# Optimization experiments

Hardware: AMD Instinct MI355X
Metric: run time of the kernel (lower is better)

Reference implementation:

```python
import jax, jax.numpy as jnp
from jax import lax
import numpy as np

K = 3        # kernel_size
G = 8        # groups
BN_EPS = 1e-5


def setup_inputs() -> dict:
    key = jax.random.key(0)
    k1, k2, k3, k4 = jax.random.split(key, 4)
    N, C, H, W = 16, 256, 128, 128
    x = jax.random.normal(k1, (N, C, H, W), dtype=jnp.float32)
    # grouped conv: out = G*K*K = 72 channels, in-per-group = C/G = 32, OIHW layout
    fan_out = (G * K * K // G) * K * K  # kaiming fan_out per torch convention
    std = np.sqrt(2.0 / fan_out)
    conv_w = jax.random.normal(k2, (G * K * K, C // G, K, K), dtype=jnp.float32) * std
    gamma = jnp.ones((G * K * K,), dtype=jnp.float32)
    beta = jnp.zeros((G * K * K,), dtype=jnp.float32)
    running_mean = jax.random.normal(k3, (G * K * K,), dtype=jnp.float32) * 0.1
    running_var = jax.random.uniform(k4, (G * K * K,), dtype=jnp.float32, minval=0.5, maxval=1.5)
    return {"x": x, "conv_w": conv_w, "gamma": gamma, "beta": beta,
            "running_mean": running_mean, "running_var": running_var}


def reference(x, conv_w, gamma, beta, running_mean, running_var):
    n, c, h, w = x.shape
    # ReflectionPad2d(K//2)
    xp = jnp.pad(x, ((0, 0), (0, 0), (1, 1), (1, 1)), mode="reflect")
    # grouped conv -> per-pixel logits, shape (n, G*K*K, h, w)
    sigma = lax.conv_general_dilated(
        xp, conv_w, window_strides=(1, 1), padding="VALID",
        dimension_numbers=("NCHW", "OIHW", "NCHW"), feature_group_count=G)
    # BatchNorm (inference mode: running stats)
    scale = gamma * lax.rsqrt(running_var + BN_EPS)
    sigma = sigma * scale[None, :, None, None] + (beta - running_mean * scale)[None, :, None, None]
    # softmax over the full channel dim (faithful to nn.Softmax(dim=1) on G*K*K channels)
    sigma = jax.nn.softmax(sigma, axis=1)
    sigma = sigma.reshape(n, G, K * K, h, w)
    # unfold(x_pad, K): 9 shifted views, channel-major then row-major kernel order
    patches = jnp.stack(
        [xp[:, :, i:i + h, j:j + w] for i in range(K) for j in range(K)], axis=2
    )  # (n, c, K*K, h, w)
    patches = patches.reshape(n, G, c // G, K * K, h, w)
    # per-pixel weighted sum over kernel taps, weights shared within each group
    out = jnp.einsum("ngpkhw,ngkhw->ngphw", patches, sigma)
    return out.reshape(n, c, h, w)
```

## Files before the change

### kernel.cpp

```cpp
#include <hip/hip_runtime.h>


#define NN    16
#define CTOT  256
#define HH    128
#define WW    128
#define NG    8
#define CPG   32
#define NCH   72
#define BN_EPS 1e-5f

typedef float f2 __attribute__((ext_vector_type(2)));

__global__ void aaf_prep(const float* __restrict__ gamma,
                         const float* __restrict__ beta,
                         const float* __restrict__ rmean,
                         const float* __restrict__ rvar,
                         float* __restrict__ ws) {
    int t = threadIdx.x;
    if (t < NCH) {
        float sc = gamma[t] * rsqrtf(rvar[t] + BN_EPS);
        ws[t]       = sc;
        ws[NCH + t] = beta[t] - rmean[t] * sc;
    }
}

__global__ __launch_bounds__(512, 4) void aaf_main(
    const float* __restrict__ x,
    const float* __restrict__ wf,
    const float* __restrict__ scale,
    const float* __restrict__ bias,
    float* __restrict__ out) {

    __shared__ float red_m[NG][WW];
    __shared__ float red_s[NG][WW];

    int t = threadIdx.x & 63;
    int g = __builtin_amdgcn_readfirstlane((int)threadIdx.x >> 6);

    int bid = blockIdx.x;
    int row = (bid & 7) * (2048 / 8) + (bid >> 3);
    int n = row >> 7;
    int h = row & 127;

    int ys[3];
    ys[0] = (h == 0)   ? 1   : h - 1;
    ys[1] = h;
    ys[2] = (h == 127) ? 126 : h + 1;

    const float* xg = x + ((size_t)n << 22) + ((size_t)(g * CPG) << 14);
    int w0 = t << 1;

    float sig0[9], sig1[9];
#pragma unroll
    for (int o = 0; o < 9; o++) { sig0[o] = 0.f; sig1[o] = 0.f; }

    for (int ci = 0; ci < CPG; ci++) {
        const float* xc = xg + ((size_t)ci << 14);
        const float* wb = wf + (size_t)(g * 9) * (CPG * 9) + ci * 9;
#pragma unroll
        for (int ky = 0; ky < 3; ky++) {
            f2 ab = *reinterpret_cast<const f2*>(xc + (ys[ky] << 7) + w0);
            float a = ab.x, b = ab.y;
            float l = __shfl_up(b, 1);
            float r = __shfl_down(a, 1);
#pragma unroll
            for (int o = 0; o < 9; o++) {
                float wk0 = wb[o * (CPG * 9) + ky * 3 + 0];
                float wk1 = wb[o * (CPG * 9) + ky * 3 + 1];
                float wk2 = wb[o * (CPG * 9) + ky * 3 + 2];
                sig0[o] = fmaf(l, wk0, fmaf(a, wk1, fmaf(b, wk2, sig0[o])));
                sig1[o] = fmaf(a, wk0, fmaf(b, wk1, fmaf(r, wk2, sig1[o])));
            }
        }
    }

    float m0 = -3.0e38f, m1 = -3.0e38f;
#pragma unroll
    for (int o = 0; o < 9; o++) {
        float sc = scale[g * 9 + o], bi = bias[g * 9 + o];
        sig0[o] = fmaf(sig0[o], sc, bi);
        sig1[o] = fmaf(sig1[o], sc, bi);
        m0 = fmaxf(m0, sig0[o]);
        m1 = fmaxf(m1, sig1[o]);
    }
    float S0 = 0.f, S1 = 0.f;
#pragma unroll
    for (int o = 0; o < 9; o++) {
        sig0[o] = __expf(sig0[o] - m0);
        sig1[o] = __expf(sig1[o] - m1);
        S0 += sig0[o];
        S1 += sig1[o];
    }
    red_m[g][w0]     = m0;
    red_m[g][w0 + 1] = m1;
    red_s[g][w0]     = S0;
    red_s[g][w0 + 1] = S1;

    __syncthreads();
    float d0 = 0.f, d1 = 0.f;
#pragma unroll
    for (int rg = 0; rg < NG; rg++) {
        d0 += red_s[rg][w0]     * __expf(red_m[rg][w0]     - m0);
        d1 += red_s[rg][w0 + 1] * __expf(red_m[rg][w0 + 1] - m1);
    }
    float inv0 = 1.f / d0, inv1 = 1.f / d1;
#pragma unroll
    for (int o = 0; o < 9; o++) { sig0[o] *= inv0; sig1[o] *= inv1; }

    size_t obase = ((size_t)n << 22) + ((size_t)(g * CPG) << 14)
                 + ((size_t)h << 7) + (size_t)w0;
    for (int ci = 0; ci < CPG; ci++) {
        const float* xc = xg + ((size_t)ci << 14);
        float o0 = 0.f, o1 = 0.f;
#pragma unroll
        for (int ky = 0; ky < 3; ky++) {
            f2 ab = *reinterpret_cast<const f2*>(xc + (ys[ky] << 7) + w0);
            float a = ab.x, b = ab.y;
            float l = __shfl_up(b, 1);
            float r = __shfl_down(a, 1);
            o0 = fmaf(l, sig0[ky * 3 + 0], fmaf(a, sig0[ky * 3 + 1], fmaf(b, sig0[ky * 3 + 2], o0)));
            o1 = fmaf(a, sig1[ky * 3 + 0], fmaf(b, sig1[ky * 3 + 1], fmaf(r, sig1[ky * 3 + 2], o1)));
        }
        f2 ov; ov.x = o0; ov.y = o1;
        __builtin_nontemporal_store(ov,
            reinterpret_cast<f2*>(out + obase + ((size_t)ci << 14)));
    }
}

extern "C" void kernel_launch(void* const* d_in, const int* in_sizes, int n_in,
                              void* d_out, int out_size, void* d_ws, size_t ws_size,
                              hipStream_t stream) {
    const float* x     = (const float*)d_in[0];
    const float* cw    = (const float*)d_in[1];
    const float* gamma = (const float*)d_in[2];
    const float* beta  = (const float*)d_in[3];
    const float* rmean = (const float*)d_in[4];
    const float* rvar  = (const float*)d_in[5];
    float* out = (float*)d_out;
    float* ws  = (float*)d_ws;

    hipLaunchKernelGGL(aaf_prep, dim3(1), dim3(128), 0, stream,
                       gamma, beta, rmean, rvar, ws);

    int blocks = NN * HH;
    hipLaunchKernelGGL(aaf_main, dim3(blocks), dim3(512), 0, stream,
                       x, cw, ws, ws + NCH, out);
}
```

Measured before the change: 545.2 us.

## Process four pixels per thread and two rows per block with float4 loads

```diff
diff --git a/kernel.cpp b/kernel.cpp
--- a/kernel.cpp
+++ b/kernel.cpp
@@ -11,6 +11,7 @@
 #define BN_EPS 1e-5f
 
 typedef float f2 __attribute__((ext_vector_type(2)));
+typedef float f4 __attribute__((ext_vector_type(4)));
 
 __global__ void aaf_prep(const float* __restrict__ gamma,
                          const float* __restrict__ beta,
@@ -32,16 +33,19 @@
     const float* __restrict__ bias,
     float* __restrict__ out) {
 
-    __shared__ float red_m[NG][WW];
-    __shared__ float red_s[NG][WW];
+    __shared__ f4 red_m[NG][64];
+    __shared__ f4 red_s[NG][64];
 
-    int t = threadIdx.x & 63;
-    int g = __builtin_amdgcn_readfirstlane((int)threadIdx.x >> 6);
+    int t  = threadIdx.x & 63;
+    int g  = __builtin_amdgcn_readfirstlane((int)threadIdx.x >> 6);
+    int half = t >> 5;
+    int tl   = t & 31;
+    int w0   = tl << 2;
 
     int bid = blockIdx.x;
-    int row = (bid & 7) * (2048 / 8) + (bid >> 3);
-    int n = row >> 7;
-    int h = row & 127;
+    int pr  = (bid & 7) * (1024 / 8) + (bid >> 3);
+    int n   = pr >> 6;
+    int h   = ((pr & 63) << 1) + half;
 
     int ys[3];
     ys[0] = (h == 0)   ? 1   : h - 1;
@@ -49,82 +53,97 @@
     ys[2] = (h == 127) ? 126 : h + 1;
 
     const float* xg = x + ((size_t)n << 22) + ((size_t)(g * CPG) << 14);
-    int w0 = t << 1;
 
-    float sig0[9], sig1[9];
+    float s0[9], s1[9], s2[9], s3[9];
 #pragma unroll
-    for (int o = 0; o < 9; o++) { sig0[o] = 0.f; sig1[o] = 0.f; }
+    for (int o = 0; o < 9; o++) { s0[o] = 0.f; s1[o] = 0.f; s2[o] = 0.f; s3[o] = 0.f; }
 
     for (int ci = 0; ci < CPG; ci++) {
         const float* xc = xg + ((size_t)ci << 14);
         const float* wb = wf + (size_t)(g * 9) * (CPG * 9) + ci * 9;
 #pragma unroll
         for (int ky = 0; ky < 3; ky++) {
-            f2 ab = *reinterpret_cast<const f2*>(xc + (ys[ky] << 7) + w0);
-            float a = ab.x, b = ab.y;
-            float l = __shfl_up(b, 1);
-            float r = __shfl_down(a, 1);
+            f4 v = *reinterpret_cast<const f4*>(xc + (ys[ky] << 7) + w0);
+            float l = __shfl_up(v.w, 1);
+            l = (tl == 0) ? v.y : l;
+            float r = __shfl_down(v.x, 1);
+            r = (tl == 31) ? v.z : r;
 #pragma unroll
             for (int o = 0; o < 9; o++) {
                 float wk0 = wb[o * (CPG * 9) + ky * 3 + 0];
                 float wk1 = wb[o * (CPG * 9) + ky * 3 + 1];
                 float wk2 = wb[o * (CPG * 9) + ky * 3 + 2];
-                sig0[o] = fmaf(l, wk0, fmaf(a, wk1, fmaf(b, wk2, sig0[o])));
-                sig1[o] = fmaf(a, wk0, fmaf(b, wk1, fmaf(r, wk2, sig1[o])));
+                s0[o] = fmaf(l,   wk0, fmaf(v.x, wk1, fmaf(v.y, wk2, s0[o])));
+                s1[o] = fmaf(v.x, wk0, fmaf(v.y, wk1, fmaf(v.z, wk2, s1[o])));
+                s2[o] = fmaf(v.y, wk0, fmaf(v.z, wk1, fmaf(v.w, wk2, s2[o])));
+                s3[o] = fmaf(v.z, wk0, fmaf(v.w, wk1, fmaf(r,   wk2, s3[o])));
             }
         }
     }
 
-    float m0 = -3.0e38f, m1 = -3.0e38f;
+    float m0 = -3.0e38f, m1 = -3.0e38f, m2 = -3.0e38f, m3 = -3.0e38f;
 #pragma unroll
     for (int o = 0; o < 9; o++) {
         float sc = scale[g * 9 + o], bi = bias[g * 9 + o];
-        sig0[o] = fmaf(sig0[o], sc, bi);
-        sig1[o] = fmaf(sig1[o], sc, bi);
-        m0 = fmaxf(m0, sig0[o]);
-        m1 = fmaxf(m1, sig1[o]);
+        s0[o] = fmaf(s0[o], sc, bi);  m0 = fmaxf(m0, s0[o]);
+        s1[o] = fmaf(s1[o], sc, bi);  m1 = fmaxf(m1, s1[o]);
+        s2[o] = fmaf(s2[o], sc, bi);  m2 = fmaxf(m2, s2[o]);
+        s3[o] = fmaf(s3[o], sc, bi);  m3 = fmaxf(m3, s3[o]);
     }
-    float S0 = 0.f, S1 = 0.f;
+    float S0 = 0.f, S1 = 0.f, S2 = 0.f, S3 = 0.f;
 #pragma unroll
     for (int o = 0; o < 9; o++) {
-        sig0[o] = __expf(sig0[o] - m0);
-        sig1[o] = __expf(sig1[o] - m1);
-        S0 += sig0[o];
-        S1 += sig1[o];
+        s0[o] = __expf(s0[o] - m0);  S0 += s0[o];
+        s1[o] = __expf(s1[o] - m1);  S1 += s1[o];
+        s2[o] = __expf(s2[o] - m2);  S2 += s2[o];
+        s3[o] = __expf(s3[o] - m3);  S3 += s3[o];
     }
-    red_m[g][w0]     = m0;
-    red_m[g][w0 + 1] = m1;
-    red_s[g][w0]     = S0;
-    red_s[g][w0 + 1] = S1;
+    {
+        f4 mm; mm.x = m0; mm.y = m1; mm.z = m2; mm.w = m3;
+        f4 ss; ss.x = S0; ss.y = S1; ss.z = S2; ss.w = S3;
+        red_m[g][t] = mm;
+        red_s[g][t] = ss;
+    }
 
     __syncthreads();
-    float d0 = 0.f, d1 = 0.f;
+    float d0 = 0.f, d1 = 0.f, d2 = 0.f, d3 = 0.f;
 #pragma unroll
     for (int rg = 0; rg < NG; rg++) {
-        d0 += red_s[rg][w0]     * __expf(red_m[rg][w0]     - m0);
-        d1 += red_s[rg][w0 + 1] * __expf(red_m[rg][w0 + 1] - m1);
+        f4 mm = red_m[rg][t];
+        f4 ss = red_s[rg][t];
+        d0 += ss.x * __expf(mm.x - m0);
+        d1 += ss.y * __expf(mm.y - m1);
+        d2 += ss.z * __expf(mm.z - m2);
+        d3 += ss.w * __expf(mm.w - m3);
     }
-    float inv0 = 1.f / d0, inv1 = 1.f / d1;
+    float i0 = 1.f / d0, i1 = 1.f / d1, i2 = 1.f / d2, i3 = 1.f / d3;
 #pragma unroll
-    for (int o = 0; o < 9; o++) { sig0[o] *= inv0; sig1[o] *= inv1; }
+    for (int o = 0; o < 9; o++) { s0[o] *= i0; s1[o] *= i1; s2[o] *= i2; s3[o] *= i3; }
 
     size_t obase = ((size_t)n << 22) + ((size_t)(g * CPG) << 14)
                  + ((size_t)h << 7) + (size_t)w0;
     for (int ci = 0; ci < CPG; ci++) {
         const float* xc = xg + ((size_t)ci << 14);
-        float o0 = 0.f, o1 = 0.f;
+        float o0 = 0.f, o1 = 0.f, o2 = 0.f, o3 = 0.f;
 #pragma unroll
         for (int ky = 0; ky < 3; ky++) {
-            f2 ab = *reinterpret_cast<const f2*>(xc + (ys[ky] << 7) + w0);
-            float a = ab.x, b = ab.y;
-            float l = __shfl_up(b, 1);
-            float r = __shfl_down(a, 1);
-            o0 = fmaf(l, sig0[ky * 3 + 0], fmaf(a, sig0[ky * 3 + 1], fmaf(b, sig0[ky * 3 + 2], o0)));
-            o1 = fmaf(a, sig1[ky * 3 + 0], fmaf(b, sig1[ky * 3 + 1], fmaf(r, sig1[ky * 3 + 2], o1)));
+            f4 v = *reinterpret_cast<const f4*>(xc + (ys[ky] << 7) + w0);
+            float l = __shfl_up(v.w, 1);
+            l = (tl == 0) ? v.y : l;
+            float r = __shfl_down(v.x, 1);
+            r = (tl == 31) ? v.z : r;
+            float e0 = s0[ky * 3 + 0], e1 = s0[ky * 3 + 1], e2 = s0[ky * 3 + 2];
+            o0 = fmaf(l,   e0, fmaf(v.x, e1, fmaf(v.y, e2, o0)));
+            e0 = s1[ky * 3 + 0]; e1 = s1[ky * 3 + 1]; e2 = s1[ky * 3 + 2];
+            o1 = fmaf(v.x, e0, fmaf(v.y, e1, fmaf(v.z, e2, o1)));
+            e0 = s2[ky * 3 + 0]; e1 = s2[ky * 3 + 1]; e2 = s2[ky * 3 + 2];
+            o2 = fmaf(v.y, e0, fmaf(v.z, e1, fmaf(v.w, e2, o2)));
+            e0 = s3[ky * 3 + 0]; e1 = s3[ky * 3 + 1]; e2 = s3[ky * 3 + 2];
+            o3 = fmaf(v.z, e0, fmaf(v.w, e1, fmaf(r,   e2, o3)));
         }
-        f2 ov; ov.x = o0; ov.y = o1;
+        f4 ov; ov.x = o0; ov.y = o1; ov.z = o2; ov.w = o3;
         __builtin_nontemporal_store(ov,
-            reinterpret_cast<f2*>(out + obase + ((size_t)ci << 14)));
+            reinterpret_cast<f4*>(out + obase + ((size_t)ci << 14)));
     }
 }
 
@@ -143,7 +162,7 @@
     hipLaunchKernelGGL(aaf_prep, dim3(1), dim3(128), 0, stream,
                        gamma, beta, rmean, rvar, ws);
 
-    int blocks = NN * HH;
+    int blocks = NN * HH / 2;
     hipLaunchKernelGGL(aaf_main, dim3(blocks), dim3(512), 0, stream,
                        x, cw, ws, ws + NCH, out);
 }
```

After: 538.9 us. No clear change (-1.1%).
